# Kernel optimization log

Measured on AMD Instinct MI355X. Metric: run time of the kernel, lower is better.

Reference implementation:

```python
import jax, jax.numpy as jnp
import numpy as np

E, B, D, H, Z = 8, 16384, 512, 512, 64   # experts, batch, input_dim, hidden, latent
NHID = 2                                 # num_mlp_layers - 1 hidden-to-hidden layers


def setup_inputs() -> dict:
    key = jax.random.key(0)
    ks = jax.random.split(key, 12)

    def w(k, shape, fan_in):
        return (jax.random.normal(k, shape, jnp.float32) / np.sqrt(fan_in)).astype(jnp.float32)

    return {
        "x": jax.random.normal(ks[0], (B, D), jnp.float32),
        "eps": jax.random.normal(ks[1], (B, Z), jnp.float32),
        # stacked per-expert parameters (leading axis E)
        "enc_in_w": w(ks[2], (E, D, H), D), "enc_in_b": jnp.zeros((E, H), jnp.float32),
        "enc_hid_w": w(ks[3], (E, NHID, H, H), H), "enc_hid_b": jnp.zeros((E, NHID, H), jnp.float32),
        "mu_w": w(ks[4], (E, H, Z), H), "mu_b": jnp.zeros((E, Z), jnp.float32),
        "lv_w": w(ks[5], (E, H, Z), H), "lv_b": jnp.zeros((E, Z), jnp.float32),
        "dec_in_w": w(ks[6], (E, Z, H), Z), "dec_in_b": jnp.zeros((E, H), jnp.float32),
        "dec_hid_w": w(ks[7], (E, NHID, H, H), H), "dec_hid_b": jnp.zeros((E, NHID, H), jnp.float32),
        "dec_out_w": w(ks[8], (E, H, D), H), "dec_out_b": jnp.zeros((E, D), jnp.float32),
    }


def _moe_forward(x, eps, enc_in_w, enc_in_b, enc_hid_w, enc_hid_b,
                 mu_w, mu_b, lv_w, lv_b,
                 dec_in_w, dec_in_b, dec_hid_w, dec_hid_b, dec_out_w, dec_out_b):
    # ---- every expert tries the problem (dense, all experts over full batch) ----
    h = jax.nn.relu(jnp.einsum('bd,edh->ebh', x, enc_in_w) + enc_in_b[:, None, :])
    for i in range(NHID):
        h = jax.nn.relu(jnp.einsum('ebh,ehk->ebk', h, enc_hid_w[:, i]) + enc_hid_b[:, i, None, :])
    mu = jnp.einsum('ebh,ehz->ebz', h, mu_w) + mu_b[:, None, :]          # [E,B,Z]
    logvar = jnp.einsum('ebh,ehz->ebz', h, lv_w) + lv_b[:, None, :]       # [E,B,Z]
    z = mu + jnp.exp(0.5 * logvar) * eps[None, :, :]                      # reparameterize
    g = jax.nn.relu(jnp.einsum('ebz,ezh->ebh', z, dec_in_w) + dec_in_b[:, None, :])
    for i in range(NHID):
        g = jax.nn.relu(jnp.einsum('ebh,ehk->ebk', g, dec_hid_w[:, i]) + dec_hid_b[:, i, None, :])
    xhat = jnp.einsum('ebh,ehd->ebd', g, dec_out_w) + dec_out_b[:, None, :]  # [E,B,D]

    # ---- per-sample recon loss, pick best expert (torch.min over experts) ----
    recon = jnp.mean((xhat - x[None, :, :]) ** 2, axis=-1)                # [E,B]
    expert_idx = jnp.argmin(recon, axis=0)                                # [B]

    # ---- sparse_others: single fused gather instead of python loop ----
    bi = jnp.arange(x.shape[0])
    return mu[expert_idx, bi], logvar[expert_idx, bi], xhat[expert_idx, bi]


def reference(x, eps, enc_in_w, enc_in_b, enc_hid_w, enc_hid_b,
              mu_w, mu_b, lv_w, lv_b,
              dec_in_w, dec_in_b, dec_hid_w, dec_hid_b, dec_out_w, dec_out_b):
    return _moe_forward(x, eps, enc_in_w, enc_in_b, enc_hid_w, enc_hid_b,
                        mu_w, mu_b, lv_w, lv_b,
                        dec_in_w, dec_in_b, dec_hid_w, dec_hid_b, dec_out_w, dec_out_b)
```

## Files before the change

### kernel.cpp

```cpp
#include <hip/hip_runtime.h>
#include <cstdint>

#define Eexp 8
#define Bb   16384
#define Dd   512
#define Hh   512
#define Zz   64

typedef _Float16 f16x8 __attribute__((ext_vector_type(8)));
typedef _Float16 f16x4 __attribute__((ext_vector_type(4)));
typedef float    f32x4 __attribute__((ext_vector_type(4)));

#define PEREXP     1671168
#define OFF_ENCIN  0
#define OFF_HID0   262144
#define OFF_HID1   524288
#define OFF_MU     786432
#define OFF_LV     819200
#define OFF_DECIN  851968
#define OFF_DHID0  884736
#define OFF_DHID1  1146880
#define OFF_DECOUT 1409024
#define WT_ELEMS   (8 * (size_t)PEREXP)

#define GLL16(g, l) __builtin_amdgcn_global_load_lds( \
    (const __attribute__((address_space(1))) void*)(g), \
    (__attribute__((address_space(3))) void*)(l), 16, 0, 0)

__global__ __launch_bounds__(256)
void tsplit(const float* __restrict__ src, _Float16* __restrict__ dH,
            _Float16* __restrict__ dL, int K, int N, long sStride, long dStride)
{
    __shared__ float t[64][65];
    const int e  = blockIdx.z;
    const int n0 = blockIdx.x * 64, k0 = blockIdx.y * 64;
    const float* S = src + (size_t)e * sStride;
    const int tid = threadIdx.x;
    const int rr = tid >> 4, cc = (tid & 15) * 4;
    #pragma unroll
    for (int p = 0; p < 4; ++p) {
        const float4 v = *reinterpret_cast<const float4*>(
            &S[(size_t)(k0 + rr + p * 16) * N + n0 + cc]);
        t[rr + p * 16][cc + 0] = v.x; t[rr + p * 16][cc + 1] = v.y;
        t[rr + p * 16][cc + 2] = v.z; t[rr + p * 16][cc + 3] = v.w;
    }
    __syncthreads();
    _Float16* DH = dH + (size_t)e * dStride;
    _Float16* DL = dL + (size_t)e * dStride;
    #pragma unroll
    for (int p = 0; p < 4; ++p) {
        const int no = rr + p * 16;
        const float a = t[cc + 0][no], b = t[cc + 1][no];
        const float c = t[cc + 2][no], d = t[cc + 3][no];
        const _Float16 ha = (_Float16)a, hb = (_Float16)b;
        const _Float16 hc = (_Float16)c, hd = (_Float16)d;
        f16x4 hv = {ha, hb, hc, hd};
        f16x4 lv = {(_Float16)(a - (float)ha), (_Float16)(b - (float)hb),
                    (_Float16)(c - (float)hc), (_Float16)(d - (float)hd)};
        *reinterpret_cast<f16x4*>(&DH[(size_t)(n0 + no) * K + k0 + cc]) = hv;
        *reinterpret_cast<f16x4*>(&DL[(size_t)(n0 + no) * K + k0 + cc]) = lv;
    }
}

__global__ __launch_bounds__(256)
void xsplit(const float4* __restrict__ src, f16x4* __restrict__ dh,
            f16x4* __restrict__ dl)
{
    const int i = blockIdx.x * 256 + threadIdx.x;
    const float4 v = src[i];
    const _Float16 h0 = (_Float16)v.x, h1 = (_Float16)v.y;
    const _Float16 h2 = (_Float16)v.z, h3 = (_Float16)v.w;
    f16x4 hv = {h0, h1, h2, h3};
    f16x4 lv = {(_Float16)(v.x - (float)h0), (_Float16)(v.y - (float)h1),
                (_Float16)(v.z - (float)h2), (_Float16)(v.w - (float)h3)};
    dh[i] = hv; dl[i] = lv;
}

template<int BN, int MODE>
__global__ __launch_bounds__(256, 2)
void gemm_sp(const _Float16* __restrict__ Ah, const _Float16* __restrict__ Al,
             const _Float16* __restrict__ Wh0, const _Float16* __restrict__ Wl0,
             const float* __restrict__ bias0,
             float* __restrict__ Cf0, _Float16* __restrict__ Ch0,
             _Float16* __restrict__ Cl0,
             const _Float16* __restrict__ Wh1, const _Float16* __restrict__ Wl1,
             const float* __restrict__ bias1, float* __restrict__ Cf1,
             int Ka, int Nout)
{
    constexpr int BM = 128, BK = 32;
    constexpr int WN = BN / 2;
    constexpr int NF = WN / 16;
    constexpr int CPW = BN / 64;
    __shared__ __align__(16) _Float16 sAh[BM * BK], sAl[BM * BK];
    __shared__ __align__(16) _Float16 sWh[BN * BK], sWl[BN * BK];

    const int nY = (MODE == 2) ? 2 : (Nout / BN);
    int wg = blockIdx.x;
    wg = (wg & 7) * (gridDim.x >> 3) + (wg >> 3);
    const int bx = wg / nY;
    const int by = wg % nY;

    const _Float16* WhP = Wh0; const _Float16* WlP = Wl0;
    const float* biasP = bias0; float* CfP = Cf0;
    if (MODE == 2 && by == 1) { WhP = Wh1; WlP = Wl1; biasP = bias1; CfP = Cf1; }

    const int tid  = threadIdx.x;
    const int lane = tid & 63;
    const int wid  = tid >> 6;
    const int wr = wid >> 1, wc = wid & 1;
    const int row0 = bx * BM;
    const int col0 = (MODE == 2) ? 0 : by * BN;

    f32x4 acc[4][NF];
    #pragma unroll
    for (int i = 0; i < 4; ++i)
        #pragma unroll
        for (int j = 0; j < NF; ++j) acc[i][j] = {0.f, 0.f, 0.f, 0.f};

    for (int k0 = 0; k0 < Ka; k0 += BK) {
        __syncthreads();
        #pragma unroll
        for (int p = 0; p < 2; ++p) {
            const int q  = wid * 2 + p;
            const int rl = q * 16 + (lane >> 2);
            const int c  = (lane & 3) ^ ((rl >> 1) & 3);
            const size_t gi = (size_t)(row0 + rl) * Ka + k0 + c * 8;
            GLL16(Ah + gi, &sAh[q * 512]);
            GLL16(Al + gi, &sAl[q * 512]);
        }
        #pragma unroll
        for (int p = 0; p < CPW; ++p) {
            const int q  = wid * CPW + p;
            const int rl = q * 16 + (lane >> 2);
            const int c  = (lane & 3) ^ ((rl >> 1) & 3);
            const size_t gi = (size_t)(col0 + rl) * Ka + k0 + c * 8;
            GLL16(WhP + gi, &sWh[q * 512]);
            GLL16(WlP + gi, &sWl[q * 512]);
        }
        __syncthreads();
        f16x8 fah[4], fal[4], fwh[NF], fwl[NF];
        #pragma unroll
        for (int mf = 0; mf < 4; ++mf) {
            const int r = wr * 64 + mf * 16 + (lane & 15);
            const int c = (lane >> 4) ^ ((r >> 1) & 3);
            const int idx = r * 32 + c * 8;
            fah[mf] = *reinterpret_cast<f16x8*>(&sAh[idx]);
            fal[mf] = *reinterpret_cast<f16x8*>(&sAl[idx]);
        }
        #pragma unroll
        for (int nf = 0; nf < NF; ++nf) {
            const int r = wc * WN + nf * 16 + (lane & 15);
            const int c = (lane >> 4) ^ ((r >> 1) & 3);
            const int idx = r * 32 + c * 8;
            fwh[nf] = *reinterpret_cast<f16x8*>(&sWh[idx]);
            fwl[nf] = *reinterpret_cast<f16x8*>(&sWl[idx]);
        }
        #pragma unroll
        for (int mf = 0; mf < 4; ++mf)
            #pragma unroll
            for (int nf = 0; nf < NF; ++nf) {
                acc[mf][nf] = __builtin_amdgcn_mfma_f32_16x16x32_f16(
                    fah[mf], fwh[nf], acc[mf][nf], 0, 0, 0);
                acc[mf][nf] = __builtin_amdgcn_mfma_f32_16x16x32_f16(
                    fah[mf], fwl[nf], acc[mf][nf], 0, 0, 0);
                acc[mf][nf] = __builtin_amdgcn_mfma_f32_16x16x32_f16(
                    fal[mf], fwh[nf], acc[mf][nf], 0, 0, 0);
            }
    }

    #pragma unroll
    for (int nf = 0; nf < NF; ++nf) {
        const int col = col0 + wc * WN + nf * 16 + (lane & 15);
        const float bv = biasP[col];
        #pragma unroll
        for (int mf = 0; mf < 4; ++mf)
            #pragma unroll
            for (int j = 0; j < 4; ++j) {
                const int rowg = row0 + wr * 64 + mf * 16 + (lane >> 4) * 4 + j;
                float v = acc[mf][nf][j] + bv;
                if (MODE == 0) {
                    v = fmaxf(v, 0.f);
                    const _Float16 h = (_Float16)v;
                    const _Float16 l = (_Float16)(v - (float)h);
                    Ch0[(size_t)rowg * Nout + col] = h;
                    Cl0[(size_t)rowg * Nout + col] = l;
                } else {
                    CfP[(size_t)rowg * Nout + col] = v;
                }
            }
    }
}

__global__ __launch_bounds__(256)
void z_kernel(const float4* __restrict__ mu, const float4* __restrict__ lv,
              const float4* __restrict__ eps, f16x4* __restrict__ zh,
              f16x4* __restrict__ zl)
{
    const int i = blockIdx.x * 256 + threadIdx.x;
    const float4 m = mu[i], l = lv[i], e = eps[i];
    float4 r;
    r.x = m.x + expf(0.5f * l.x) * e.x;
    r.y = m.y + expf(0.5f * l.y) * e.y;
    r.z = m.z + expf(0.5f * l.z) * e.z;
    r.w = m.w + expf(0.5f * l.w) * e.w;
    const _Float16 h0 = (_Float16)r.x, h1 = (_Float16)r.y;
    const _Float16 h2 = (_Float16)r.z, h3 = (_Float16)r.w;
    f16x4 hv = {h0, h1, h2, h3};
    f16x4 lvv = {(_Float16)(r.x - (float)h0), (_Float16)(r.y - (float)h1),
                 (_Float16)(r.z - (float)h2), (_Float16)(r.w - (float)h3)};
    zh[i] = hv; zl[i] = lvv;
}

__global__ __launch_bounds__(256)
void recon_kernel(const float* __restrict__ xhat, const float* __restrict__ x,
                  float* __restrict__ recon)
{
    const int wave = threadIdx.x >> 6;
    const int lane = threadIdx.x & 63;
    const int row  = blockIdx.x * 4 + wave;
    const float4* xh = reinterpret_cast<const float4*>(&xhat[(size_t)row * Dd]);
    const float4* xx = reinterpret_cast<const float4*>(&x[(size_t)row * Dd]);
    float s = 0.f;
    #pragma unroll
    for (int it = 0; it < 2; ++it) {
        const float4 a = xh[lane + it * 64];
        const float4 b = xx[lane + it * 64];
        float d;
        d = a.x - b.x; s = fmaf(d, d, s);
        d = a.y - b.y; s = fmaf(d, d, s);
        d = a.z - b.z; s = fmaf(d, d, s);
        d = a.w - b.w; s = fmaf(d, d, s);
    }
    #pragma unroll
    for (int off = 32; off > 0; off >>= 1) s += __shfl_down(s, off);
    if (lane == 0) recon[row] = s * (1.0f / 512.0f);
}

__global__ __launch_bounds__(256)
void select_kernel(const float* __restrict__ recon, float* __restrict__ best,
                   const float* __restrict__ mu_e, const float* __restrict__ lv_e,
                   const float* __restrict__ xhat,
                   float* __restrict__ out_mu, float* __restrict__ out_lv,
                   float* __restrict__ out_xh, int isFirst)
{
    const int wave = threadIdx.x >> 6;
    const int lane = threadIdx.x & 63;
    const int row  = blockIdx.x * 4 + wave;
    const float r  = recon[row];
    const bool cond = isFirst || (r < best[row]);
    if (cond) {
        if (lane == 0) best[row] = r;
        out_mu[(size_t)row * Zz + lane] = mu_e[(size_t)row * Zz + lane];
        out_lv[(size_t)row * Zz + lane] = lv_e[(size_t)row * Zz + lane];
        const float4* src = reinterpret_cast<const float4*>(&xhat[(size_t)row * Dd]);
        float4*       dst = reinterpret_cast<float4*>(&out_xh[(size_t)row * Dd]);
        dst[lane]      = src[lane];
        dst[lane + 64] = src[lane + 64];
    }
}

extern "C" void kernel_launch(void* const* d_in, const int* in_sizes, int n_in,
                              void* d_out, int out_size, void* d_ws, size_t ws_size,
                              hipStream_t stream)
{
    const float* x         = (const float*)d_in[0];
    const float* eps       = (const float*)d_in[1];
    const float* enc_in_w  = (const float*)d_in[2];
    const float* enc_in_b  = (const float*)d_in[3];
    const float* enc_hid_w = (const float*)d_in[4];
    const float* enc_hid_b = (const float*)d_in[5];
    const float* mu_w      = (const float*)d_in[6];
    const float* mu_b      = (const float*)d_in[7];
    const float* lv_w      = (const float*)d_in[8];
    const float* lv_b      = (const float*)d_in[9];
    const float* dec_in_w  = (const float*)d_in[10];
    const float* dec_in_b  = (const float*)d_in[11];
    const float* dec_hid_w = (const float*)d_in[12];
    const float* dec_hid_b = (const float*)d_in[13];
    const float* dec_out_w = (const float*)d_in[14];
    const float* dec_out_b = (const float*)d_in[15];

    const size_t BD = (size_t)Bb * 512;
    const size_t BZ = (size_t)Bb * 64;

    _Float16* wtH = (_Float16*)d_ws;
    _Float16* wtL = wtH + WT_ELEMS;
    _Float16* xh  = wtL + WT_ELEMS;
    _Float16* xl  = xh + BD;
    _Float16* aH  = xl + BD;
    _Float16* aL  = aH + BD;
    _Float16* bH  = aL + BD;
    _Float16* bL  = bH + BD;
    _Float16* zh  = bL + BD;
    _Float16* zl  = zh + BZ;
    float* fbase  = (float*)(zl + BZ);
    float* xhat   = fbase;
    float* mu_e   = xhat + BD;
    float* lv_e   = mu_e + BZ;
    float* rec    = lv_e + BZ;
    float* best   = rec + Bb;

    float* out_mu = (float*)d_out;
    float* out_lv = out_mu + (size_t)Bb * Zz;
    float* out_xh = out_lv + (size_t)Bb * Zz;

    const dim3 blk(256);

    tsplit<<<dim3(8, 8, 8), blk, 0, stream>>>(enc_in_w,           wtH + OFF_ENCIN,  wtL + OFF_ENCIN,  512, 512, 262144, PEREXP);
    tsplit<<<dim3(8, 8, 8), blk, 0, stream>>>(enc_hid_w,          wtH + OFF_HID0,   wtL + OFF_HID0,   512, 512, 524288, PEREXP);
    tsplit<<<dim3(8, 8, 8), blk, 0, stream>>>(enc_hid_w + 262144, wtH + OFF_HID1,   wtL + OFF_HID1,   512, 512, 524288, PEREXP);
    tsplit<<<dim3(1, 8, 8), blk, 0, stream>>>(mu_w,               wtH + OFF_MU,     wtL + OFF_MU,     512,  64,  32768, PEREXP);
    tsplit<<<dim3(1, 8, 8), blk, 0, stream>>>(lv_w,               wtH + OFF_LV,     wtL + OFF_LV,     512,  64,  32768, PEREXP);
    tsplit<<<dim3(8, 1, 8), blk, 0, stream>>>(dec_in_w,           wtH + OFF_DECIN,  wtL + OFF_DECIN,   64, 512,  32768, PEREXP);
    tsplit<<<dim3(8, 8, 8), blk, 0, stream>>>(dec_hid_w,          wtH + OFF_DHID0,  wtL + OFF_DHID0,  512, 512, 524288, PEREXP);
    tsplit<<<dim3(8, 8, 8), blk, 0, stream>>>(dec_hid_w + 262144, wtH + OFF_DHID1,  wtL + OFF_DHID1,  512, 512, 524288, PEREXP);
    tsplit<<<dim3(8, 8, 8), blk, 0, stream>>>(dec_out_w,          wtH + OFF_DECOUT, wtL + OFF_DECOUT, 512, 512, 262144, PEREXP);
    xsplit<<<dim3(BD / 4 / 256), blk, 0, stream>>>(
        (const float4*)x, (f16x4*)xh, (f16x4*)xl);

    const dim3 gBig(512);
    const dim3 gDual(256);
    const dim3 gRow(Bb / 4);
    const dim3 gZ(BZ / 4 / 256);

    for (int e = 0; e < Eexp; ++e) {
        const size_t wo = (size_t)e * PEREXP;
        gemm_sp<128, 0><<<gBig, blk, 0, stream>>>(
            xh, xl, wtH + wo + OFF_ENCIN, wtL + wo + OFF_ENCIN,
            enc_in_b + (size_t)e * Hh, nullptr, aH, aL,
            nullptr, nullptr, nullptr, nullptr, Dd, Hh);
        gemm_sp<128, 0><<<gBig, blk, 0, stream>>>(
            aH, aL, wtH + wo + OFF_HID0, wtL + wo + OFF_HID0,
            enc_hid_b + ((size_t)e * 2 + 0) * Hh, nullptr, bH, bL,
            nullptr, nullptr, nullptr, nullptr, Hh, Hh);
        gemm_sp<128, 0><<<gBig, blk, 0, stream>>>(
            bH, bL, wtH + wo + OFF_HID1, wtL + wo + OFF_HID1,
            enc_hid_b + ((size_t)e * 2 + 1) * Hh, nullptr, aH, aL,
            nullptr, nullptr, nullptr, nullptr, Hh, Hh);
        gemm_sp<64, 2><<<gDual, blk, 0, stream>>>(
            aH, aL, wtH + wo + OFF_MU, wtL + wo + OFF_MU,
            mu_b + (size_t)e * Zz, mu_e, nullptr, nullptr,
            wtH + wo + OFF_LV, wtL + wo + OFF_LV,
            lv_b + (size_t)e * Zz, lv_e, Hh, Zz);
        z_kernel<<<gZ, blk, 0, stream>>>(
            (const float4*)mu_e, (const float4*)lv_e, (const float4*)eps,
            (f16x4*)zh, (f16x4*)zl);
        gemm_sp<128, 0><<<gBig, blk, 0, stream>>>(
            zh, zl, wtH + wo + OFF_DECIN, wtL + wo + OFF_DECIN,
            dec_in_b + (size_t)e * Hh, nullptr, bH, bL,
            nullptr, nullptr, nullptr, nullptr, Zz, Hh);
        gemm_sp<128, 0><<<gBig, blk, 0, stream>>>(
            bH, bL, wtH + wo + OFF_DHID0, wtL + wo + OFF_DHID0,
            dec_hid_b + ((size_t)e * 2 + 0) * Hh, nullptr, aH, aL,
            nullptr, nullptr, nullptr, nullptr, Hh, Hh);
        gemm_sp<128, 0><<<gBig, blk, 0, stream>>>(
            aH, aL, wtH + wo + OFF_DHID1, wtL + wo + OFF_DHID1,
            dec_hid_b + ((size_t)e * 2 + 1) * Hh, nullptr, bH, bL,
            nullptr, nullptr, nullptr, nullptr, Hh, Hh);
        gemm_sp<128, 1><<<gBig, blk, 0, stream>>>(
            bH, bL, wtH + wo + OFF_DECOUT, wtL + wo + OFF_DECOUT,
            dec_out_b + (size_t)e * Dd, xhat, nullptr, nullptr,
            nullptr, nullptr, nullptr, nullptr, Hh, Dd);
        recon_kernel<<<gRow, blk, 0, stream>>>(xhat, x, rec);
        select_kernel<<<gRow, blk, 0, stream>>>(
            rec, best, mu_e, lv_e, xhat, out_mu, out_lv, out_xh, e == 0 ? 1 : 0);
    }
}
```

Before: 2.060 ms.

## Double-buffer GEMM LDS, switch to 32x32 MFMA, fuse recon loss into output GEMM

```diff
diff --git a/kernel.cpp b/kernel.cpp
--- a/kernel.cpp
+++ b/kernel.cpp
@@ -7,9 +7,9 @@
 #define Hh   512
 #define Zz   64
 
-typedef _Float16 f16x8 __attribute__((ext_vector_type(8)));
-typedef _Float16 f16x4 __attribute__((ext_vector_type(4)));
-typedef float    f32x4 __attribute__((ext_vector_type(4)));
+typedef _Float16 f16x8  __attribute__((ext_vector_type(8)));
+typedef _Float16 f16x4  __attribute__((ext_vector_type(4)));
+typedef float    f32x16 __attribute__((ext_vector_type(16)));
 
 #define PEREXP     1671168
 #define OFF_ENCIN  0
@@ -85,14 +85,15 @@
              _Float16* __restrict__ Cl0,
              const _Float16* __restrict__ Wh1, const _Float16* __restrict__ Wl1,
              const float* __restrict__ bias1, float* __restrict__ Cf1,
+             const float* __restrict__ Xin, float* __restrict__ rec8,
              int Ka, int Nout)
 {
     constexpr int BM = 128, BK = 32;
     constexpr int WN = BN / 2;
-    constexpr int NF = WN / 16;
+    constexpr int NF = WN / 32;
     constexpr int CPW = BN / 64;
-    __shared__ __align__(16) _Float16 sAh[BM * BK], sAl[BM * BK];
-    __shared__ __align__(16) _Float16 sWh[BN * BK], sWl[BN * BK];
+    __shared__ __align__(16) _Float16 sA[2][2][BM * BK];
+    __shared__ __align__(16) _Float16 sW[2][2][BN * BK];
 
     const int nY = (MODE == 2) ? 2 : (Nout / BN);
     int wg = blockIdx.x;
@@ -111,73 +112,97 @@
     const int row0 = bx * BM;
     const int col0 = (MODE == 2) ? 0 : by * BN;
 
-    f32x4 acc[4][NF];
-    #pragma unroll
-    for (int i = 0; i < 4; ++i)
+    f32x16 acc[2][NF];
+    #pragma unroll
+    for (int i = 0; i < 2; ++i)
         #pragma unroll
-        for (int j = 0; j < NF; ++j) acc[i][j] = {0.f, 0.f, 0.f, 0.f};
-
-    for (int k0 = 0; k0 < Ka; k0 += BK) {
-        __syncthreads();
+        for (int j = 0; j < NF; ++j)
+            #pragma unroll
+            for (int r = 0; r < 16; ++r) acc[i][j][r] = 0.f;
+
+    const int clane = lane >> 2;
+    const int cslot = lane & 3;
+
+    #define STAGE(buf, k0)                                                  \
+    {                                                                       \
+        _Pragma("unroll")                                                   \
+        for (int p = 0; p < 2; ++p) {                                       \
+            const int q  = wid * 2 + p;                                     \
+            const int rl = q * 16 + clane;                                  \
+            const int c  = cslot ^ ((rl >> 1) & 3);                         \
+            const size_t gi = (size_t)(row0 + rl) * Ka + (k0) + c * 8;      \
+            GLL16(Ah + gi, &sA[buf][0][q * 512]);                           \
+            GLL16(Al + gi, &sA[buf][1][q * 512]);                           \
+        }                                                                   \
+        _Pragma("unroll")                                                   \
+        for (int p = 0; p < CPW; ++p) {                                     \
+            const int q  = wid * CPW + p;                                   \
+            const int rl = q * 16 + clane;                                  \
+            const int c  = cslot ^ ((rl >> 1) & 3);                         \
+            const size_t gi = (size_t)(col0 + rl) * Ka + (k0) + c * 8;      \
+            GLL16(WhP + gi, &sW[buf][0][q * 512]);                          \
+            GLL16(WlP + gi, &sW[buf][1][q * 512]);                          \
+        }                                                                   \
+    }
+
+    STAGE(0, 0)
+    asm volatile("s_waitcnt vmcnt(0)" ::: "memory");
+    __builtin_amdgcn_s_barrier();
+
+    const int NT = Ka / BK;
+    int cur = 0;
+    for (int t = 0; t < NT; ++t) {
+        if (t + 1 < NT) STAGE(cur ^ 1, (t + 1) * BK)
+
         #pragma unroll
-        for (int p = 0; p < 2; ++p) {
-            const int q  = wid * 2 + p;
-            const int rl = q * 16 + (lane >> 2);
-            const int c  = (lane & 3) ^ ((rl >> 1) & 3);
-            const size_t gi = (size_t)(row0 + rl) * Ka + k0 + c * 8;
-            GLL16(Ah + gi, &sAh[q * 512]);
-            GLL16(Al + gi, &sAl[q * 512]);
+        for (int kk = 0; kk < 2; ++kk) {
+            f16x8 fah[2], fal[2], fwh[NF], fwl[NF];
+            #pragma unroll
+            for (int mf = 0; mf < 2; ++mf) {
+                const int r = wr * 64 + mf * 32 + (lane & 31);
+                const int u = ((lane >> 5) + 2 * kk) ^ ((r >> 1) & 3);
+                fah[mf] = *reinterpret_cast<f16x8*>(&sA[cur][0][r * 32 + u * 8]);
+                fal[mf] = *reinterpret_cast<f16x8*>(&sA[cur][1][r * 32 + u * 8]);
+            }
+            #pragma unroll
+            for (int nf = 0; nf < NF; ++nf) {
+                const int r = wc * WN + nf * 32 + (lane & 31);
+                const int u = ((lane >> 5) + 2 * kk) ^ ((r >> 1) & 3);
+                fwh[nf] = *reinterpret_cast<f16x8*>(&sW[cur][0][r * 32 + u * 8]);
+                fwl[nf] = *reinterpret_cast<f16x8*>(&sW[cur][1][r * 32 + u * 8]);
+            }
+            __builtin_amdgcn_s_setprio(1);
+            #pragma unroll
+            for (int mf = 0; mf < 2; ++mf)
+                #pragma unroll
+                for (int nf = 0; nf < NF; ++nf) {
+                    acc[mf][nf] = __builtin_amdgcn_mfma_f32_32x32x16_f16(
+                        fah[mf], fwh[nf], acc[mf][nf], 0, 0, 0);
+                    acc[mf][nf] = __builtin_amdgcn_mfma_f32_32x32x16_f16(
+                        fah[mf], fwl[nf], acc[mf][nf], 0, 0, 0);
+                    acc[mf][nf] = __builtin_amdgcn_mfma_f32_32x32x16_f16(
+                        fal[mf], fwh[nf], acc[mf][nf], 0, 0, 0);
+                }
+            __builtin_amdgcn_s_setprio(0);
         }
-        #pragma unroll
-        for (int p = 0; p < CPW; ++p) {
-            const int q  = wid * CPW + p;
-            const int rl = q * 16 + (lane >> 2);
-            const int c  = (lane & 3) ^ ((rl >> 1) & 3);
-            const size_t gi = (size_t)(col0 + rl) * Ka + k0 + c * 8;
-            GLL16(WhP + gi, &sWh[q * 512]);
-            GLL16(WlP + gi, &sWl[q * 512]);
-        }
-        __syncthreads();
-        f16x8 fah[4], fal[4], fwh[NF], fwl[NF];
-        #pragma unroll
-        for (int mf = 0; mf < 4; ++mf) {
-            const int r = wr * 64 + mf * 16 + (lane & 15);
-            const int c = (lane >> 4) ^ ((r >> 1) & 3);
-            const int idx = r * 32 + c * 8;
-            fah[mf] = *reinterpret_cast<f16x8*>(&sAh[idx]);
-            fal[mf] = *reinterpret_cast<f16x8*>(&sAl[idx]);
-        }
-        #pragma unroll
-        for (int nf = 0; nf < NF; ++nf) {
-            const int r = wc * WN + nf * 16 + (lane & 15);
-            const int c = (lane >> 4) ^ ((r >> 1) & 3);
-            const int idx = r * 32 + c * 8;
-            fwh[nf] = *reinterpret_cast<f16x8*>(&sWh[idx]);
-            fwl[nf] = *reinterpret_cast<f16x8*>(&sWl[idx]);
-        }
-        #pragma unroll
-        for (int mf = 0; mf < 4; ++mf)
-            #pragma unroll
-            for (int nf = 0; nf < NF; ++nf) {
-                acc[mf][nf] = __builtin_amdgcn_mfma_f32_16x16x32_f16(
-                    fah[mf], fwh[nf], acc[mf][nf], 0, 0, 0);
-                acc[mf][nf] = __builtin_amdgcn_mfma_f32_16x16x32_f16(
-                    fah[mf], fwl[nf], acc[mf][nf], 0, 0, 0);
-                acc[mf][nf] = __builtin_amdgcn_mfma_f32_16x16x32_f16(
-                    fal[mf], fwh[nf], acc[mf][nf], 0, 0, 0);
-            }
-    }
+        asm volatile("s_waitcnt vmcnt(0)" ::: "memory");
+        __builtin_amdgcn_s_barrier();
+        cur ^= 1;
+    }
+    #undef STAGE
 
     #pragma unroll
     for (int nf = 0; nf < NF; ++nf) {
-        const int col = col0 + wc * WN + nf * 16 + (lane & 15);
+        const int col = col0 + wc * WN + nf * 32 + (lane & 31);
         const float bv = biasP[col];
         #pragma unroll
-        for (int mf = 0; mf < 4; ++mf)
-            #pragma unroll
-            for (int j = 0; j < 4; ++j) {
-                const int rowg = row0 + wr * 64 + mf * 16 + (lane >> 4) * 4 + j;
-                float v = acc[mf][nf][j] + bv;
+        for (int mf = 0; mf < 2; ++mf) {
+            float sse[16];
+            #pragma unroll
+            for (int rg = 0; rg < 16; ++rg) {
+                const int rloc = (rg & 3) + 8 * (rg >> 2) + 4 * (lane >> 5);
+                const int rowg = row0 + wr * 64 + mf * 32 + rloc;
+                float v = acc[mf][nf][rg] + bv;
                 if (MODE == 0) {
                     v = fmaxf(v, 0.f);
                     const _Float16 h = (_Float16)v;
@@ -186,17 +211,39 @@
                     Cl0[(size_t)rowg * Nout + col] = l;
                 } else {
                     CfP[(size_t)rowg * Nout + col] = v;
+                    if (MODE == 1) {
+                        const float d = v - Xin[(size_t)rowg * Nout + col];
+                        sse[rg] = d * d;
+                    }
                 }
             }
+            if (MODE == 1) {
+                #pragma unroll
+                for (int rg = 0; rg < 16; ++rg) {
+                    float s = sse[rg];
+                    #pragma unroll
+                    for (int m = 1; m < 32; m <<= 1) s += __shfl_xor(s, m);
+                    if ((lane & 31) == 0) {
+                        const int rloc = (rg & 3) + 8 * (rg >> 2) + 4 * (lane >> 5);
+                        const int rowg = row0 + wr * 64 + mf * 32 + rloc;
+                        if (nf == 0)
+                            rec8[(size_t)(by * 2 + wc) * Bb + rowg] = s;
+                        else
+                            rec8[(size_t)(by * 2 + wc) * Bb + rowg] += s;
+                    }
+                }
+            }
+        }
     }
 }
 
 __global__ __launch_bounds__(256)
 void z_kernel(const float4* __restrict__ mu, const float4* __restrict__ lv,
               const float4* __restrict__ eps, f16x4* __restrict__ zh,
-              f16x4* __restrict__ zl)
+              f16x4* __restrict__ zl, float* __restrict__ rec8)
 {
     const int i = blockIdx.x * 256 + threadIdx.x;
+    if (i < Eexp * Bb) rec8[i] = 0.f;
     const float4 m = mu[i], l = lv[i], e = eps[i];
     float4 r;
     r.x = m.x + expf(0.5f * l.x) * e.x;
@@ -212,32 +259,7 @@
 }
 
 __global__ __launch_bounds__(256)
-void recon_kernel(const float* __restrict__ xhat, const float* __restrict__ x,
-                  float* __restrict__ recon)
-{
-    const int wave = threadIdx.x >> 6;
-    const int lane = threadIdx.x & 63;
-    const int row  = blockIdx.x * 4 + wave;
-    const float4* xh = reinterpret_cast<const float4*>(&xhat[(size_t)row * Dd]);
-    const float4* xx = reinterpret_cast<const float4*>(&x[(size_t)row * Dd]);
-    float s = 0.f;
-    #pragma unroll
-    for (int it = 0; it < 2; ++it) {
-        const float4 a = xh[lane + it * 64];
-        const float4 b = xx[lane + it * 64];
-        float d;
-        d = a.x - b.x; s = fmaf(d, d, s);
-        d = a.y - b.y; s = fmaf(d, d, s);
-        d = a.z - b.z; s = fmaf(d, d, s);
-        d = a.w - b.w; s = fmaf(d, d, s);
-    }
-    #pragma unroll
-    for (int off = 32; off > 0; off >>= 1) s += __shfl_down(s, off);
-    if (lane == 0) recon[row] = s * (1.0f / 512.0f);
-}
-
-__global__ __launch_bounds__(256)
-void select_kernel(const float* __restrict__ recon, float* __restrict__ best,
+void select_kernel(const float* __restrict__ rec8, float* __restrict__ best,
                    const float* __restrict__ mu_e, const float* __restrict__ lv_e,
                    const float* __restrict__ xhat,
                    float* __restrict__ out_mu, float* __restrict__ out_lv,
@@ -246,7 +268,10 @@
     const int wave = threadIdx.x >> 6;
     const int lane = threadIdx.x & 63;
     const int row  = blockIdx.x * 4 + wave;
-    const float r  = recon[row];
+    float r = 0.f;
+    #pragma unroll
+    for (int p = 0; p < 8; ++p) r += rec8[(size_t)p * Bb + row];
+    r *= (1.0f / 512.0f);
     const bool cond = isFirst || (r < best[row]);
     if (cond) {
         if (lane == 0) best[row] = r;
@@ -297,8 +322,8 @@
     float* xhat   = fbase;
     float* mu_e   = xhat + BD;
     float* lv_e   = mu_e + BZ;
-    float* rec    = lv_e + BZ;
-    float* best   = rec + Bb;
+    float* rec8   = lv_e + BZ;
+    float* best   = rec8 + (size_t)Eexp * Bb;
 
     float* out_mu = (float*)d_out;
     float* out_lv = out_mu + (size_t)Bb * Zz;
@@ -328,41 +353,40 @@
         gemm_sp<128, 0><<<gBig, blk, 0, stream>>>(
             xh, xl, wtH + wo + OFF_ENCIN, wtL + wo + OFF_ENCIN,
             enc_in_b + (size_t)e * Hh, nullptr, aH, aL,
-            nullptr, nullptr, nullptr, nullptr, Dd, Hh);
+            nullptr, nullptr, nullptr, nullptr, nullptr, nullptr, Dd, Hh);
         gemm_sp<128, 0><<<gBig, blk, 0, stream>>>(
             aH, aL, wtH + wo + OFF_HID0, wtL + wo + OFF_HID0,
             enc_hid_b + ((size_t)e * 2 + 0) * Hh, nullptr, bH, bL,
-            nullptr, nullptr, nullptr, nullptr, Hh, Hh);
+            nullptr, nullptr, nullptr, nullptr, nullptr, nullptr, Hh, Hh);
         gemm_sp<128, 0><<<gBig, blk, 0, stream>>>(
             bH, bL, wtH + wo + OFF_HID1, wtL + wo + OFF_HID1,
             enc_hid_b + ((size_t)e * 2 + 1) * Hh, nullptr, aH, aL,
-            nullptr, nullptr, nullptr, nullptr, Hh, Hh);
+            nullptr, nullptr, nullptr, nullptr, nullptr, nullptr, Hh, Hh);
         gemm_sp<64, 2><<<gDual, blk, 0, stream>>>(
             aH, aL, wtH + wo + OFF_MU, wtL + wo + OFF_MU,
             mu_b + (size_t)e * Zz, mu_e, nullptr, nullptr,
             wtH + wo + OFF_LV, wtL + wo + OFF_LV,
-            lv_b + (size_t)e * Zz, lv_e, Hh, Zz);
+            lv_b + (size_t)e * Zz, lv_e, nullptr, nullptr, Hh, Zz);
         z_kernel<<<gZ, blk, 0, stream>>>(
             (const float4*)mu_e, (const float4*)lv_e, (const float4*)eps,
-            (f16x4*)zh, (f16x4*)zl);
+            (f16x4*)zh, (f16x4*)zl, rec8);
         gemm_sp<128, 0><<<gBig, blk, 0, stream>>>(
             zh, zl, wtH + wo + OFF_DECIN, wtL + wo + OFF_DECIN,
             dec_in_b + (size_t)e * Hh, nullptr, bH, bL,
-            nullptr, nullptr, nullptr, nullptr, Zz, Hh);
+            nullptr, nullptr, nullptr, nullptr, nullptr, nullptr, Zz, Hh);
         gemm_sp<128, 0><<<gBig, blk, 0, stream>>>(
             bH, bL, wtH + wo + OFF_DHID0, wtL + wo + OFF_DHID0,
             dec_hid_b + ((size_t)e * 2 + 0) * Hh, nullptr, aH, aL,
-            nullptr, nullptr, nullptr, nullptr, Hh, Hh);
+            nullptr, nullptr, nullptr, nullptr, nullptr, nullptr, Hh, Hh);
         gemm_sp<128, 0><<<gBig, blk, 0, stream>>>(
             aH, aL, wtH + wo + OFF_DHID1, wtL + wo + OFF_DHID1,
             dec_hid_b + ((size_t)e * 2 + 1) * Hh, nullptr, bH, bL,
-            nullptr, nullptr, nullptr, nullptr, Hh, Hh);
+            nullptr, nullptr, nullptr, nullptr, nullptr, nullptr, Hh, Hh);
         gemm_sp<128, 1><<<gBig, blk, 0, stream>>>(
             bH, bL, wtH + wo + OFF_DECOUT, wtL + wo + OFF_DECOUT,
             dec_out_b + (size_t)e * Dd, xhat, nullptr, nullptr,
-            nullptr, nullptr, nullptr, nullptr, Hh, Dd);
-        recon_kernel<<<gRow, blk, 0, stream>>>(xhat, x, rec);
+            nullptr, nullptr, nullptr, nullptr, x, rec8, Hh, Dd);
         select_kernel<<<gRow, blk, 0, stream>>>(
-            rec, best, mu_e, lv_e, xhat, out_mu, out_lv, out_xh, e == 0 ? 1 : 0);
-    }
-}
+            rec8, best, mu_e, lv_e, xhat, out_mu, out_lv, out_xh, e == 0 ? 1 : 0);
+    }
+}
```

Result: slower. 2.182 ms (+5.9%).
